# Optimization experiments

Hardware: AMD Instinct MI355X
Metric: run time of the kernel (lower is better)

## Reference

```python
import jax, jax.numpy as jnp
import numpy as np

B, S, I = 16, 512, 64
D, H, L, F = 512, 8, 6, 2048
MAX_REL = 32
EPS = 1e-5


def setup_inputs() -> dict:
    key = jax.random.key(0)
    ks = jax.random.split(key, 16)
    sc = 0.02
    inp = {
        "x": jax.random.normal(ks[0], (B, S, I), dtype=jnp.float32),
        "in_W": jax.random.normal(ks[1], (I, D), dtype=jnp.float32) * sc,
        "in_b": jnp.zeros((D,), jnp.float32),
        "rel_emb": jax.random.normal(ks[2], (2 * MAX_REL + 1, D), dtype=jnp.float32) * sc,
        "qkvo_W": jax.random.normal(ks[3], (L, 4, D, D), dtype=jnp.float32) * sc,
        "qkvo_b": jnp.zeros((L, 4, D), jnp.float32),
        "ln_g": jnp.ones((L, 2, D), jnp.float32),
        "ln_b": jnp.zeros((L, 2, D), jnp.float32),
        "ff_W1": jax.random.normal(ks[4], (L, D, F), dtype=jnp.float32) * sc,
        "ff_b1": jnp.zeros((L, F), jnp.float32),
        "ff_W2": jax.random.normal(ks[5], (L, F, D), dtype=jnp.float32) * sc,
        "ff_b2": jnp.zeros((L, D), jnp.float32),
        "out_W": jax.random.normal(ks[6], (D, 1), dtype=jnp.float32) * sc,
        "out_b": jnp.zeros((1,), jnp.float32),
    }
    return inp


def _layernorm(x, g, b):
    mu = jnp.mean(x, axis=-1, keepdims=True)
    var = jnp.mean((x - mu) ** 2, axis=-1, keepdims=True)
    return (x - mu) * jax.lax.rsqrt(var + EPS) * g + b


def reference(x, in_W, in_b, rel_emb, qkvo_W, qkvo_b, ln_g, ln_b, ff_W1, ff_b1, ff_W2, ff_b2, out_W, out_b):
    b, s, _ = x.shape
    dk = D // H
    h = x @ in_W + in_b  # (B,S,D)
    # relative positional encoding: mean over query axis of gathered embeddings
    pos = jnp.arange(s)
    rel = jnp.clip(pos[:, None] - pos[None, :], -MAX_REL, MAX_REL) + MAX_REL  # (S,S)
    rp = rel_emb[rel]  # (S,S,D)
    h = h + rp.mean(axis=0)[None]  # broadcast over batch

    def layer(h, p):
        Wqkvo, bqkvo, g, bl, W1, b1, W2, b2 = p
        def proj(i):
            return (h @ Wqkvo[i] + bqkvo[i]).reshape(b, s, H, dk).transpose(0, 2, 1, 3)
        q, k, v = proj(0), proj(1), proj(2)  # (B,H,S,dk)
        scores = jnp.einsum("bhqd,bhkd->bhqk", q, k) / jnp.sqrt(jnp.float32(dk))
        attn = jax.nn.softmax(scores, axis=-1)
        ctx = jnp.einsum("bhqk,bhkd->bhqd", attn, v)
        ctx = ctx.transpose(0, 2, 1, 3).reshape(b, s, D)
        ao = ctx @ Wqkvo[3] + bqkvo[3]
        h1 = _layernorm(h + ao, g[0], bl[0])
        ff = jax.nn.relu(h1 @ W1 + b1) @ W2 + b2
        h2 = _layernorm(h1 + ff, g[1], bl[1])
        return h2, None

    h, _ = jax.lax.scan(layer, h, (qkvo_W, qkvo_b, ln_g, ln_b, ff_W1, ff_b1, ff_W2, ff_b2))
    out = h @ out_W + out_b  # (B,S,1)
    return out
```

## Files before the change

kernel.cpp:

```cpp
#include <hip/hip_runtime.h>
#include <math.h>

#define B 16
#define S 512
#define IN 64
#define D 512
#define H 8
#define DK 64
#define L 6
#define F 2048
#define BS (B*S)
#define EPS 1e-5f

typedef short short8 __attribute__((ext_vector_type(8)));
typedef short short4v __attribute__((ext_vector_type(4)));
typedef float floatx4 __attribute__((ext_vector_type(4)));

static __device__ inline short f2bf(float x) {
    unsigned u = __float_as_uint(x);
    unsigned r = (u + 0x7fffu + ((u >> 16) & 1u)) >> 16;
    return (short)r;
}
static __device__ inline float bf2f(short s) {
    return __uint_as_float(((unsigned)(unsigned short)s) << 16);
}

__global__ __launch_bounds__(256) void pe_kernel(const float* __restrict__ rel_emb,
                                                 float* __restrict__ pe) {
    int k = blockIdx.x;
    int d = threadIdx.x;
    float acc0 = 0.f, acc1 = 0.f;
    for (int r = 0; r < 65; ++r) {
        float w;
        if (r == 0)       w = (float)max(0, k - 31);
        else if (r == 64) w = (float)max(0, S - (k + 32));
        else {
            int qpos = k + r - 32;
            w = (qpos >= 0 && qpos < S) ? 1.f : 0.f;
        }
        acc0 += w * rel_emb[r * D + d];
        acc1 += w * rel_emb[r * D + d + 256];
    }
    pe[k * D + d]       = acc0 * (1.f / (float)S);
    pe[k * D + d + 256] = acc1 * (1.f / (float)S);
}

__global__ __launch_bounds__(256) void wtrans_kernel(const float* __restrict__ src,
                                                     short* __restrict__ dst,
                                                     int K, int N) {
    __shared__ float Ls[32][33];
    const int z = blockIdx.z, kb = blockIdx.y, nb = blockIdx.x;
    const int tx = threadIdx.x & 31, ty = threadIdx.x >> 5;
    src += (size_t)z * K * N;
    dst += (size_t)z * K * N;
#pragma unroll
    for (int i = 0; i < 4; ++i)
        Ls[ty + i * 8][tx] = src[(size_t)(kb * 32 + ty + i * 8) * N + nb * 32 + tx];
    __syncthreads();
#pragma unroll
    for (int i = 0; i < 4; ++i) {
        int n = nb * 32 + ty + i * 8;
        dst[(size_t)n * K + kb * 32 + tx] = f2bf(Ls[tx][ty + i * 8]);
    }
}

__global__ __launch_bounds__(256) void cvt_kernel(const float* __restrict__ in,
                                                  short* __restrict__ out) {
    int i = (blockIdx.x * 256 + threadIdx.x) * 4;
    float4 v = *(const float4*)(in + i);
    short4v o;
    o.x = f2bf(v.x); o.y = f2bf(v.y); o.z = f2bf(v.z); o.w = f2bf(v.w);
    *(short4v*)(out + i) = o;
}

__global__ __launch_bounds__(256) void vtrans_kernel(const short* __restrict__ v,
                                                     short* __restrict__ vt) {
    __shared__ short Ls[64 * 72];
    const int bh = blockIdx.y, jt = blockIdx.x * 64;
    const int t = threadIdx.x;
    const int r = t >> 2, cg = t & 3;
    *(short8*)&Ls[r * 72 + cg * 8] =
        *(const short8*)(v + ((size_t)bh * S + jt + r) * DK + cg * 8);
    *(short8*)&Ls[r * 72 + 32 + cg * 8] =
        *(const short8*)(v + ((size_t)bh * S + jt + r) * DK + 32 + cg * 8);
    __syncthreads();
    const int d = t >> 2, sg = t & 3;
    short tmp[16];
#pragma unroll
    for (int i = 0; i < 16; ++i) tmp[i] = Ls[(sg * 16 + i) * 72 + d];
    short* dst = vt + ((size_t)bh * DK + d) * S + jt + sg * 16;
    *(short8*)(dst)     = *(short8*)&tmp[0];
    *(short8*)(dst + 8) = *(short8*)&tmp[8];
}

#define GLL(SRC, DST) __builtin_amdgcn_global_load_lds( \
    (const __attribute__((address_space(1))) void*)(SRC), \
    (__attribute__((address_space(3))) void*)(DST), 16, 0, 0)

__global__ __launch_bounds__(256) void mfma_gemm(
    const short* __restrict__ A, const short* __restrict__ Bt,
    const float* __restrict__ bias, short* __restrict__ Cb,
    float* __restrict__ Cf, int M, int N, int K, int lda, int ldb, int mode,
    const float* __restrict__ pe, long az, long wz, long bz, long cz)
{
    __shared__ short As[2][128 * 32];
    __shared__ short Bs[2][128 * 32];

    const int z = blockIdx.z;
    const short* Az = A  + (size_t)z * az;
    const short* Bz = Bt + (size_t)z * wz;

    const int t = threadIdx.x;
    const int w = t >> 6, lane = t & 63;
    const int wm = w >> 1, wn = w & 1;
    const int ln15 = lane & 15, lq = lane >> 4;
    const int bm = blockIdx.y, bn = blockIdx.x;

    const int ml = lane >> 2;
    const int kb = ((lane & 3) - (ml >> 1)) & 3;
    const short* Ag0 = Az + (size_t)(bm * 128 + w * 16 + ml)       * lda + kb * 8;
    const short* Ag1 = Az + (size_t)(bm * 128 + (w + 4) * 16 + ml) * lda + kb * 8;
    const short* Bg0 = Bz + (size_t)(bn * 128 + w * 16 + ml)       * ldb + kb * 8;
    const short* Bg1 = Bz + (size_t)(bn * 128 + (w + 4) * 16 + ml) * ldb + kb * 8;
    const int so0 = w * 512, so1 = (w + 4) * 512;

    floatx4 acc[4][4] = {};
    const int slot = ln15 * 4 + ((lq + (ln15 >> 1)) & 3);

    GLL(Ag0, &As[0][so0]);
    GLL(Ag1, &As[0][so1]);
    GLL(Bg0, &Bs[0][so0]);
    GLL(Bg1, &Bs[0][so1]);

    int buf = 0;
    for (int kt = 0; kt < K; kt += 32) {
        __syncthreads();
        const int ktn = kt + 32;
        if (ktn < K) {
            GLL(Ag0 + ktn, &As[buf ^ 1][so0]);
            GLL(Ag1 + ktn, &As[buf ^ 1][so1]);
            GLL(Bg0 + ktn, &Bs[buf ^ 1][so0]);
            GLL(Bg1 + ktn, &Bs[buf ^ 1][so1]);
        }
        short8 af[4], bf[4];
#pragma unroll
        for (int mt = 0; mt < 4; ++mt) {
            af[mt] = *(const short8*)&As[buf][((wm * 4 + mt) * 64 + slot) * 8];
            bf[mt] = *(const short8*)&Bs[buf][((wn * 4 + mt) * 64 + slot) * 8];
        }
#pragma unroll
        for (int mt = 0; mt < 4; ++mt)
#pragma unroll
            for (int nt = 0; nt < 4; ++nt)
                acc[mt][nt] = __builtin_amdgcn_mfma_f32_16x16x32_bf16(
                    af[mt], bf[nt], acc[mt][nt], 0, 0, 0);
        buf ^= 1;
    }

    short* Cbz = Cb + (size_t)z * cz;
    float* Cfz = Cf + (size_t)z * cz;
    const float* bb = bias + (size_t)z * bz;
#pragma unroll
    for (int mt = 0; mt < 4; ++mt) {
#pragma unroll
        for (int nt = 0; nt < 4; ++nt) {
            const int col = bn * 128 + wn * 64 + nt * 16 + ln15;
            const int row0 = bm * 128 + wm * 64 + mt * 16 + lq * 4;
            const float bc = (mode == 4) ? 0.f : bb[col];
#pragma unroll
            for (int reg = 0; reg < 4; ++reg) {
                const int r = row0 + reg;
                float v = acc[mt][nt][reg] + bc;
                if (mode == 4) {
                    Cfz[(size_t)r * N + col] = v;
                } else if (mode == 3) {
                    const int bi = r >> 9, si = r & (S - 1);
                    const int hh = col >> 6, dd = col & 63;
                    Cbz[(((size_t)(bi * H + hh) * S + si) * DK + dd)] = f2bf(v);
                } else {
                    if (mode == 1) v = fmaxf(v, 0.f);
                    else if (mode == 2) v += pe[(size_t)(r & (S - 1)) * D + col];
                    Cb[(size_t)r * N + col] = f2bf(v);
                }
            }
        }
    }
}

__global__ __launch_bounds__(256) void attn_mfma(
    const short* __restrict__ qg, const short* __restrict__ kg,
    const short* __restrict__ vtg, short* __restrict__ ctx)
{
    __shared__ short Ks[64 * 72];
    __shared__ short Vs[64 * 72];
    __shared__ short Ps[4][16 * 72];

    const int t = threadIdx.x;
    const int w = t >> 6, lane = t & 63;
    const int ln15 = lane & 15, lq = lane >> 4;
    const int bh = blockIdx.y, bi = bh >> 3, hh = bh & 7;
    const int qbase = blockIdx.x * 64 + w * 16;

    short8 qf0, qf1;
    {
        const short* qrow = qg + ((size_t)bh * S + qbase + ln15) * DK;
        qf0 = *(const short8*)(qrow + lq * 8);
        qf1 = *(const short8*)(qrow + 32 + lq * 8);
    }
    floatx4 o[4] = {};
    float mrow[4] = {-1e30f, -1e30f, -1e30f, -1e30f};
    float lrow[4] = {};

    const int sr = t >> 2, scg = t & 3;
    const short* kbase = kg  + (size_t)bh * S * DK;
    const short* vtb   = vtg + (size_t)bh * DK * S;

    for (int jt = 0; jt < S; jt += 64) {
        __syncthreads();
        *(short8*)&Ks[sr * 72 + scg * 8] =
            *(const short8*)(kbase + (size_t)(jt + sr) * DK + scg * 8);
        *(short8*)&Ks[sr * 72 + 32 + scg * 8] =
            *(const short8*)(kbase + (size_t)(jt + sr) * DK + 32 + scg * 8);
        *(short8*)&Vs[sr * 72 + scg * 8] =
            *(const short8*)(vtb + (size_t)sr * S + jt + scg * 8);
        *(short8*)&Vs[sr * 72 + 32 + scg * 8] =
            *(const short8*)(vtb + (size_t)sr * S + jt + 32 + scg * 8);
        __syncthreads();

        floatx4 sc[4];
#pragma unroll
        for (int nt = 0; nt < 4; ++nt) {
            floatx4 s4 = {};
            short8 kf0 = *(const short8*)&Ks[(nt * 16 + ln15) * 72 + lq * 8];
            short8 kf1 = *(const short8*)&Ks[(nt * 16 + ln15) * 72 + 32 + lq * 8];
            s4 = __builtin_amdgcn_mfma_f32_16x16x32_bf16(qf0, kf0, s4, 0, 0, 0);
            s4 = __builtin_amdgcn_mfma_f32_16x16x32_bf16(qf1, kf1, s4, 0, 0, 0);
#pragma unroll
            for (int r = 0; r < 4; ++r) s4[r] *= 0.125f;
            sc[nt] = s4;
        }

        float rmax[4];
#pragma unroll
        for (int r = 0; r < 4; ++r)
            rmax[r] = fmaxf(fmaxf(sc[0][r], sc[1][r]), fmaxf(sc[2][r], sc[3][r]));
#pragma unroll
        for (int off = 1; off < 16; off <<= 1)
#pragma unroll
            for (int r = 0; r < 4; ++r)
                rmax[r] = fmaxf(rmax[r], __shfl_xor(rmax[r], off));

        float mnew[4], alpha[4], psum[4];
#pragma unroll
        for (int r = 0; r < 4; ++r) {
            mnew[r]  = fmaxf(mrow[r], rmax[r]);
            alpha[r] = __expf(mrow[r] - mnew[r]);
            psum[r]  = 0.f;
        }
#pragma unroll
        for (int nt = 0; nt < 4; ++nt)
#pragma unroll
            for (int r = 0; r < 4; ++r) {
                float p = __expf(sc[nt][r] - mnew[r]);
                psum[r] += p;
                Ps[w][(lq * 4 + r) * 72 + nt * 16 + ln15] = f2bf(p);
            }
#pragma unroll
        for (int off = 1; off < 16; off <<= 1)
#pragma unroll
            for (int r = 0; r < 4; ++r)
                psum[r] += __shfl_xor(psum[r], off);
#pragma unroll
        for (int r = 0; r < 4; ++r) {
            lrow[r] = lrow[r] * alpha[r] + psum[r];
            mrow[r] = mnew[r];
        }
#pragma unroll
        for (int dv = 0; dv < 4; ++dv)
#pragma unroll
            for (int r = 0; r < 4; ++r)
                o[dv][r] *= alpha[r];

        short8 pf0 = *(const short8*)&Ps[w][ln15 * 72 + lq * 8];
        short8 pf1 = *(const short8*)&Ps[w][ln15 * 72 + 32 + lq * 8];
#pragma unroll
        for (int dv = 0; dv < 4; ++dv) {
            short8 vf0 = *(const short8*)&Vs[(dv * 16 + ln15) * 72 + lq * 8];
            short8 vf1 = *(const short8*)&Vs[(dv * 16 + ln15) * 72 + 32 + lq * 8];
            o[dv] = __builtin_amdgcn_mfma_f32_16x16x32_bf16(pf0, vf0, o[dv], 0, 0, 0);
            o[dv] = __builtin_amdgcn_mfma_f32_16x16x32_bf16(pf1, vf1, o[dv], 0, 0, 0);
        }
    }

    float inv[4];
#pragma unroll
    for (int r = 0; r < 4; ++r) inv[r] = 1.f / lrow[r];
#pragma unroll
    for (int dv = 0; dv < 4; ++dv)
#pragma unroll
        for (int r = 0; r < 4; ++r) {
            const int s = qbase + lq * 4 + r;
            const int col = hh * DK + dv * 16 + ln15;
            ctx[((size_t)bi * S + s) * D + col] = f2bf(o[dv][r] * inv[r]);
        }
}

__global__ __launch_bounds__(128) void ln_res_kernel(
    const short* __restrict__ a, const float* __restrict__ p0,
    const float* __restrict__ p1, const float* __restrict__ eb,
    const float* __restrict__ g, const float* __restrict__ beta,
    short* __restrict__ outb)
{
    const int row = blockIdx.x;
    const int t = threadIdx.x;
    const size_t off = (size_t)row * D + t * 4;
    const short4v xa = *(const short4v*)(a + off);
    const float4 q0 = *(const float4*)(p0 + off);
    const float4 q1 = *(const float4*)(p1 + off);
    const float4 bb2 = *(const float4*)(eb + t * 4);
    float x0 = bf2f(xa.x) + q0.x + q1.x + bb2.x;
    float x1 = bf2f(xa.y) + q0.y + q1.y + bb2.y;
    float x2 = bf2f(xa.z) + q0.z + q1.z + bb2.z;
    float x3 = bf2f(xa.w) + q0.w + q1.w + bb2.w;
    float s  = x0 + x1 + x2 + x3;
    float s2 = x0 * x0 + x1 * x1 + x2 * x2 + x3 * x3;
#pragma unroll
    for (int o = 32; o > 0; o >>= 1) {
        s  += __shfl_down(s, o);
        s2 += __shfl_down(s2, o);
    }
    __shared__ float red[2][2];
    const int wave = t >> 6;
    if ((t & 63) == 0) { red[wave][0] = s; red[wave][1] = s2; }
    __syncthreads();
    s  = red[0][0] + red[1][0];
    s2 = red[0][1] + red[1][1];
    const float mu  = s * (1.f / (float)D);
    const float var = s2 * (1.f / (float)D) - mu * mu;
    const float r   = rsqrtf(var + EPS);
    const float4 gg = *(const float4*)(g    + t * 4);
    const float4 bb = *(const float4*)(beta + t * 4);
    short4v ob;
    ob.x = f2bf((x0 - mu) * r * gg.x + bb.x);
    ob.y = f2bf((x1 - mu) * r * gg.y + bb.y);
    ob.z = f2bf((x2 - mu) * r * gg.z + bb.z);
    ob.w = f2bf((x3 - mu) * r * gg.w + bb.w);
    *(short4v*)(outb + off) = ob;
}

__global__ __launch_bounds__(256) void out_kernel(
    const short* __restrict__ h, const float* __restrict__ ow,
    const float* __restrict__ ob, float* __restrict__ out)
{
    const int wave = threadIdx.x >> 6;
    const int lane = threadIdx.x & 63;
    const int row  = blockIdx.x * 4 + wave;
    const short* hp = h + (size_t)row * D;
    float s = 0.f;
#pragma unroll
    for (int u = 0; u < 8; ++u) {
        int d = lane + u * 64;
        s += bf2f(hp[d]) * ow[d];
    }
#pragma unroll
    for (int o = 32; o > 0; o >>= 1) s += __shfl_down(s, o);
    if (lane == 0) out[row] = s + ob[0];
}

extern "C" void kernel_launch(void* const* d_in, const int* in_sizes, int n_in,
                              void* d_out, int out_size, void* d_ws, size_t ws_size,
                              hipStream_t stream) {
    const float* x       = (const float*)d_in[0];
    const float* in_W    = (const float*)d_in[1];
    const float* in_b    = (const float*)d_in[2];
    const float* rel_emb = (const float*)d_in[3];
    const float* qkvo_W  = (const float*)d_in[4];
    const float* qkvo_b  = (const float*)d_in[5];
    const float* ln_g    = (const float*)d_in[6];
    const float* ln_bb   = (const float*)d_in[7];
    const float* ff_W1   = (const float*)d_in[8];
    const float* ff_b1   = (const float*)d_in[9];
    const float* ff_W2   = (const float*)d_in[10];
    const float* ff_b2   = (const float*)d_in[11];
    const float* out_W   = (const float*)d_in[12];
    const float* out_b   = (const float*)d_in[13];
    float* out = (float*)d_out;

    const size_t HSZ = (size_t)BS * D;
    float* pe     = (float*)d_ws;
    float* part0  = pe + (size_t)S * D;
    float* part1  = part0 + HSZ;
    short* h_bf   = (short*)(part1 + HSZ);
    short* h1_bf  = h_bf  + HSZ;
    short* qkv_bf = h1_bf + HSZ;
    short* xb     = qkv_bf + 4 * HSZ;
    short* wt_qkvo = xb + (size_t)BS * IN;
    short* wt_ff1  = wt_qkvo + (size_t)L * 4 * D * D;
    short* wt_ff2  = wt_ff1  + (size_t)L * D * F;
    short* wt_in   = wt_ff2  + (size_t)L * F * D;

    const size_t CZ = (size_t)B * H * S * DK;
    short* qb = qkv_bf;
    short* kb = qkv_bf + CZ;
    short* vb = qkv_bf + 2 * CZ;
    short* vt = qkv_bf + 3 * CZ;
    short* ctx_bf = vb;
    short* ff1_bf = qkv_bf;

    dim3 blk(256);

    pe_kernel<<<dim3(S), blk, 0, stream>>>(rel_emb, pe);
    cvt_kernel<<<dim3(BS * IN / 1024), blk, 0, stream>>>(x, xb);
    wtrans_kernel<<<dim3(D / 32, IN / 32, 1), blk, 0, stream>>>(in_W, wt_in, IN, D);
    wtrans_kernel<<<dim3(D / 32, D / 32, 4 * L), blk, 0, stream>>>(qkvo_W, wt_qkvo, D, D);
    wtrans_kernel<<<dim3(F / 32, D / 32, L), blk, 0, stream>>>(ff_W1, wt_ff1, D, F);
    wtrans_kernel<<<dim3(D / 32, F / 32, L), blk, 0, stream>>>(ff_W2, wt_ff2, F, D);

    mfma_gemm<<<dim3(D / 128, BS / 128, 1), blk, 0, stream>>>(
        xb, wt_in, in_b, h_bf, nullptr, BS, D, IN, IN, IN, 2, pe, 0, 0, 0, 0);

    for (int l = 0; l < L; ++l) {
        const float* bl = qkvo_b + (size_t)l * 4 * D;
        mfma_gemm<<<dim3(D / 128, BS / 128, 3), blk, 0, stream>>>(
            h_bf, wt_qkvo + (size_t)l * 4 * D * D, bl, qkv_bf, nullptr,
            BS, D, D, D, D, 3, nullptr, 0, (long)D * D, (long)D, (long)CZ);
        vtrans_kernel<<<dim3(S / 64, B * H), blk, 0, stream>>>(vb, vt);
        attn_mfma<<<dim3(S / 64, B * H), blk, 0, stream>>>(qb, kb, vt, ctx_bf);
        mfma_gemm<<<dim3(D / 128, BS / 128, 2), blk, 0, stream>>>(
            ctx_bf, wt_qkvo + (size_t)(l * 4 + 3) * D * D, nullptr, nullptr, part0,
            BS, D, 256, D, D, 4, nullptr, 256, 256, 0, (long)HSZ);
        ln_res_kernel<<<dim3(BS), dim3(128), 0, stream>>>(
            h_bf, part0, part1, bl + 3 * D,
            ln_g + (size_t)l * 2 * D, ln_bb + (size_t)l * 2 * D, h1_bf);
        mfma_gemm<<<dim3(F / 128, BS / 128, 1), blk, 0, stream>>>(
            h1_bf, wt_ff1 + (size_t)l * D * F, ff_b1 + (size_t)l * F, ff1_bf, nullptr,
            BS, F, D, D, D, 1, nullptr, 0, 0, 0, 0);
        mfma_gemm<<<dim3(D / 128, BS / 128, 2), blk, 0, stream>>>(
            ff1_bf, wt_ff2 + (size_t)l * F * D, nullptr, nullptr, part0,
            BS, D, 1024, F, F, 4, nullptr, 1024, 1024, 0, (long)HSZ);
        ln_res_kernel<<<dim3(BS), dim3(128), 0, stream>>>(
            h1_bf, part0, part1, ff_b2 + (size_t)l * D,
            ln_g + (size_t)l * 2 * D + D, ln_bb + (size_t)l * 2 * D + D, h_bf);
    }

    out_kernel<<<dim3(BS / 4), blk, 0, stream>>>(h_bf, out_W, out_b, out);
}
```

Baseline: 1.231 ms.

## Triple-buffer GEMM LDS tiles with partial vmcnt waits to prefetch two stages ahead

Replaces the double-buffered K loop of the bf16 MFMA GEMM with a three-stage LDS ring. The loop is unrolled by three and uses explicit s_waitcnt with vmcnt 4, so the next tile's global-to-LDS loads can stay in flight while the current tile is consumed. The aim is to hide global load latency behind MFMA work instead of draining all loads at every barrier. In exchange it uses 50% more LDS, which may reduce occupancy, and it depends on hand-encoded waitcnt values being correct.

```diff
diff --git a/kernel.cpp b/kernel.cpp
--- a/kernel.cpp
+++ b/kernel.cpp
@@ -97,14 +97,40 @@
     (const __attribute__((address_space(1))) void*)(SRC), \
     (__attribute__((address_space(3))) void*)(DST), 16, 0, 0)
 
+#define SWAIT4 __builtin_amdgcn_s_waitcnt(0x0F74)
+#define SWAIT0 __builtin_amdgcn_s_waitcnt(0x0F70)
+
+#define KITER(CUR_A, CUR_B, NXT_A, NXT_B, I)                              \
+  {                                                                       \
+    if ((I) + 1 < niter) SWAIT4; else SWAIT0;                             \
+    __builtin_amdgcn_s_barrier();                                         \
+    const int kn_ = ((I) + 2) << 5;                                       \
+    if (kn_ < K) {                                                        \
+      GLL(Ag0 + kn_, NXT_A + so0); GLL(Ag1 + kn_, NXT_A + so1);           \
+      GLL(Bg0 + kn_, NXT_B + so0); GLL(Bg1 + kn_, NXT_B + so1);           \
+    }                                                                     \
+    short8 af_[4], bf_[4];                                                \
+    _Pragma("unroll")                                                     \
+    for (int mt = 0; mt < 4; ++mt) {                                      \
+      af_[mt] = *(const short8*)&CUR_A[((wm * 4 + mt) * 64 + slot) * 8];  \
+      bf_[mt] = *(const short8*)&CUR_B[((wn * 4 + mt) * 64 + slot) * 8];  \
+    }                                                                     \
+    _Pragma("unroll")                                                     \
+    for (int mt = 0; mt < 4; ++mt)                                        \
+      _Pragma("unroll")                                                   \
+      for (int nt = 0; nt < 4; ++nt)                                      \
+        acc[mt][nt] = __builtin_amdgcn_mfma_f32_16x16x32_bf16(            \
+            af_[mt], bf_[nt], acc[mt][nt], 0, 0, 0);                      \
+  }
+
 __global__ __launch_bounds__(256) void mfma_gemm(
     const short* __restrict__ A, const short* __restrict__ Bt,
     const float* __restrict__ bias, short* __restrict__ Cb,
     float* __restrict__ Cf, int M, int N, int K, int lda, int ldb, int mode,
     const float* __restrict__ pe, long az, long wz, long bz, long cz)
 {
-    __shared__ short As[2][128 * 32];
-    __shared__ short Bs[2][128 * 32];
+    __shared__ short As0[4096], As1[4096], As2[4096];
+    __shared__ short Bs0[4096], Bs1[4096], Bs2[4096];
 
     const int z = blockIdx.z;
     const short* Az = A  + (size_t)z * az;
@@ -126,36 +152,23 @@
 
     floatx4 acc[4][4] = {};
     const int slot = ln15 * 4 + ((lq + (ln15 >> 1)) & 3);
-
-    GLL(Ag0, &As[0][so0]);
-    GLL(Ag1, &As[0][so1]);
-    GLL(Bg0, &Bs[0][so0]);
-    GLL(Bg1, &Bs[0][so1]);
-
-    int buf = 0;
-    for (int kt = 0; kt < K; kt += 32) {
-        __syncthreads();
-        const int ktn = kt + 32;
-        if (ktn < K) {
-            GLL(Ag0 + ktn, &As[buf ^ 1][so0]);
-            GLL(Ag1 + ktn, &As[buf ^ 1][so1]);
-            GLL(Bg0 + ktn, &Bs[buf ^ 1][so0]);
-            GLL(Bg1 + ktn, &Bs[buf ^ 1][so1]);
-        }
-        short8 af[4], bf[4];
-#pragma unroll
-        for (int mt = 0; mt < 4; ++mt) {
-            af[mt] = *(const short8*)&As[buf][((wm * 4 + mt) * 64 + slot) * 8];
-            bf[mt] = *(const short8*)&Bs[buf][((wn * 4 + mt) * 64 + slot) * 8];
-        }
-#pragma unroll
-        for (int mt = 0; mt < 4; ++mt)
-#pragma unroll
-            for (int nt = 0; nt < 4; ++nt)
-                acc[mt][nt] = __builtin_amdgcn_mfma_f32_16x16x32_bf16(
-                    af[mt], bf[nt], acc[mt][nt], 0, 0, 0);
-        buf ^= 1;
-    }
+    const int niter = K >> 5;
+
+    GLL(Ag0, As0 + so0); GLL(Ag1, As0 + so1);
+    GLL(Bg0, Bs0 + so0); GLL(Bg1, Bs0 + so1);
+    if (niter > 1) {
+        GLL(Ag0 + 32, As1 + so0); GLL(Ag1 + 32, As1 + so1);
+        GLL(Bg0 + 32, Bs1 + so0); GLL(Bg1 + 32, Bs1 + so1);
+    }
+
+    int i = 0;
+    for (; i + 3 <= niter; i += 3) {
+        KITER(As0, Bs0, As2, Bs2, i);
+        KITER(As1, Bs1, As0, Bs0, i + 1);
+        KITER(As2, Bs2, As1, Bs1, i + 2);
+    }
+    if (i < niter)     KITER(As0, Bs0, As2, Bs2, i);
+    if (i + 1 < niter) KITER(As1, Bs1, As0, Bs0, i + 1);
 
     short* Cbz = Cb + (size_t)z * cz;
     float* Cfz = Cf + (size_t)z * cz;
```

New measurement: 1.267 ms. 1.03x slower.
